# Kernel tuning notes

Measured on AMD Instinct MI355X. Metric: run time of the kernel, lower is better.

Reference implementation:

```python
import jax, jax.numpy as jnp
import numpy as np
from jax import lax

B, T = 64, 2048
ENC, DEC, ATT = 512, 1024, 128
NFILT, KSIZE = 32, 31
PAD = KSIZE // 2


def setup_inputs() -> dict:
    key = jax.random.key(0)
    ks = jax.random.split(key, 9)
    query = jax.random.normal(ks[0], (B, 1, DEC), dtype=jnp.float32)
    keys = jax.random.normal(ks[1], (B, T, ENC), dtype=jnp.float32)
    prev_weights = jax.random.uniform(ks[2], (B, T), dtype=jnp.float32)
    mask = jax.random.randint(ks[3], (B, T), 0, 2, dtype=jnp.int32)
    # params stored as [in, out] (transpose of torch Linear weight); same math
    W1 = jax.random.normal(ks[4], (ENC, ATT), dtype=jnp.float32) * (ENC ** -0.5)
    W2 = jax.random.normal(ks[5], (DEC, ATT), dtype=jnp.float32) * (DEC ** -0.5)
    V = jax.random.normal(ks[6], (ATT,), dtype=jnp.float32) * (ATT ** -0.5)
    conv_w = jax.random.normal(ks[7], (NFILT, 1, KSIZE), dtype=jnp.float32) * (KSIZE ** -0.5)
    loc_dense = jax.random.normal(ks[8], (NFILT, ATT), dtype=jnp.float32) * (NFILT ** -0.5)
    return {"query": query, "keys": keys, "prev_weights": prev_weights, "mask": mask,
            "W1": W1, "W2": W2, "V": V, "conv_w": conv_w, "loc_dense": loc_dense}


def reference(query, keys, prev_weights, mask, W1, W2, V, conv_w, loc_dense):
    proj_key = jnp.einsum('bte,ea->bta', keys, W1)          # [B,T,A]
    proj_query = jnp.einsum('bqd,da->bqa', query, W2)       # [B,1,A]
    # location conv: input [B,1,T], kernel [F,1,K], 'same' padding -> [B,F,T]
    loc_feat = lax.conv_general_dilated(prev_weights[:, None, :], conv_w,
                                        window_strides=(1,), padding=[(PAD, PAD)],
                                        dimension_numbers=('NCH', 'OIH', 'NCH'))
    proj_loc = jnp.einsum('bft,fa->bta', loc_feat, loc_dense)  # [B,T,A]
    scores = jnp.einsum('bta,a->bt', jnp.tanh(proj_key + proj_query + proj_loc), V)
    scores = jnp.where(mask == 0, -1e9, scores)
    weights = jax.nn.softmax(scores, axis=-1)                # [B,T]
    context = jnp.einsum('bt,bte->be', weights, keys)[:, None, :]  # [B,1,ENC]
    return context, weights
```

## Files before the change

kernel.cpp:

```cpp
#include <hip/hip_runtime.h>

typedef __attribute__((ext_vector_type(4))) float f32x4;
typedef __attribute__((ext_vector_type(8))) short bf16x8;

#define T_LEN 2048
#define ENC   512
#define DEC   1024
#define ATT   128
#define NB    64
#define BM    256
#define NTB   (T_LEN / BM)
#define NSTEP 17

typedef unsigned int u32;
typedef __attribute__((address_space(1))) const u32 gu32;
typedef __attribute__((address_space(3))) u32 lu32;

__device__ __forceinline__ void async_copy16(const void* g, void* l) {
  __builtin_amdgcn_global_load_lds((gu32*)g, (lu32*)l, 16, 0, 0);
}

__device__ __forceinline__ unsigned short f2bf_rne(float x) {
  unsigned int u = __builtin_bit_cast(unsigned int, x);
  u += 0x7fff + ((u >> 16) & 1);
  return (unsigned short)(u >> 16);
}
__device__ __forceinline__ short f2bf_fast(float x) {
  unsigned int u = __builtin_bit_cast(unsigned int, x);
  return (short)((u + 0x8000u) >> 16);
}

__device__ __forceinline__ float fast_tanh(float x) {
  float e = __expf(2.f * x);
  return 1.f - 2.f / (e + 1.f);
}

__global__ __launch_bounds__(128) void prep(
    const float* __restrict__ query, const float* __restrict__ W2,
    const float* __restrict__ W1, const float* __restrict__ convw,
    const float* __restrict__ ldense,
    float* __restrict__ pq, unsigned short* __restrict__ Bl) {
  int bidx = blockIdx.x;
  if (bidx < NB) {
    int a = threadIdx.x;
    const float* q = query + bidx * DEC;
    float a0 = 0.f, a1 = 0.f, a2 = 0.f, a3 = 0.f;
    for (int d = 0; d < DEC; d += 4) {
      a0 += q[d]     * W2[(d)     * ATT + a];
      a1 += q[d + 1] * W2[(d + 1) * ATT + a];
      a2 += q[d + 2] * W2[(d + 2) * ATT + a];
      a3 += q[d + 3] * W2[(d + 3) * ATT + a];
    }
    pq[bidx * ATT + a] = (a0 + a1) + (a2 + a3);
  } else {
    int a = bidx - NB;
    int n = a >> 4, rs = a & 15;
    for (int k = threadIdx.x; k < NSTEP * 32; k += 128) {
      float v = 0.f;
      if (k < 512) {
        v = W1[k * ATT + a];
      } else if (k < 543) {
        int kc = k - 512;
        #pragma unroll
        for (int f = 0; f < 32; ++f) v += convw[f * 31 + kc] * ldense[f * ATT + a];
      }
      int t = k >> 5, g = (k & 31) >> 3, j = k & 7;
      Bl[(((t * 8 + n) * 64 + g * 16 + rs) << 3) + j] = f2bf_rne(v);
    }
  }
}

__global__ __launch_bounds__(512, 2) void lsa_main(
    const float* __restrict__ keys, const float* __restrict__ prev,
    const int* __restrict__ mask, const unsigned short* __restrict__ Bl,
    const float* __restrict__ pq, const float* __restrict__ Vv,
    float* __restrict__ wout, float* __restrict__ dpart, float* __restrict__ cpart) {
  __shared__ unsigned short Bsh[NSTEP * 4096];
  __shared__ float e_vals[BM];

  const int tid = threadIdx.x;
  const int bid = blockIdx.x;
  const int b = bid >> 3;
  const int trow0 = (bid & 7) * BM;
  const int lane = tid & 63;
  const int w = tid >> 6;
  const int rsel = lane & 15, grp = lane >> 4;
  const int row0 = trow0 + w * 32;

  const float* keyrow = keys + ((size_t)b * T_LEN + row0 + rsel) * ENC + grp * 8;

  f32x4 acc[2][8];
  #pragma unroll
  for (int m = 0; m < 2; ++m)
    #pragma unroll
    for (int n = 0; n < 8; ++n) acc[m][n] = (f32x4)0.f;

  f32x4 aP[2][2], aQ[2][2];
  #pragma unroll
  for (int m = 0; m < 2; ++m) {
    aP[m][0] = *(const f32x4*)(keyrow + m * 16 * ENC);
    aP[m][1] = *(const f32x4*)(keyrow + m * 16 * ENC + 4);
  }
  {
    const char* src = (const char*)Bl + w * 1024 + lane * 16;
    char* dst = (char*)Bsh + w * 1024;
    #pragma unroll
    for (int s = 0; s < NSTEP; ++s)
      async_copy16(src + s * 8192, dst + s * 8192);
  }
  __syncthreads();

  #pragma unroll
  for (int t = 0; t < NSTEP; ++t) {
    f32x4 (&cur)[2][2] = (t & 1) ? aQ : aP;
    f32x4 (&nxt)[2][2] = (t & 1) ? aP : aQ;
    if (t < NSTEP - 2) {
      #pragma unroll
      for (int m = 0; m < 2; ++m) {
        nxt[m][0] = *(const f32x4*)(keyrow + m * 16 * ENC + (t + 1) * 32);
        nxt[m][1] = *(const f32x4*)(keyrow + m * 16 * ENC + (t + 1) * 32 + 4);
      }
    } else if (t == NSTEP - 2) {
      #pragma unroll
      for (int m = 0; m < 2; ++m)
        #pragma unroll
        for (int h = 0; h < 2; ++h)
          #pragma unroll
          for (int j = 0; j < 4; ++j) {
            int kk = grp * 8 + h * 4 + j;
            int pos = row0 + m * 16 + rsel + kk - 15;
            nxt[m][h][j] = (kk < 31 && pos >= 0 && pos < T_LEN) ? prev[b * T_LEN + pos] : 0.f;
          }
    }
    __builtin_amdgcn_sched_barrier(0);
    bf16x8 af[2];
    #pragma unroll
    for (int m = 0; m < 2; ++m)
      #pragma unroll
      for (int j = 0; j < 4; ++j) {
        af[m][j]     = f2bf_fast(cur[m][0][j]);
        af[m][4 + j] = f2bf_fast(cur[m][1][j]);
      }
    const unsigned short* Bt = &Bsh[t * 4096];
    #pragma unroll
    for (int n = 0; n < 8; ++n) {
      bf16x8 bf = *(const bf16x8*)(Bt + n * 512 + lane * 8);
      acc[0][n] = __builtin_amdgcn_mfma_f32_16x16x32_bf16(af[0], bf, acc[0][n], 0, 0, 0);
      acc[1][n] = __builtin_amdgcn_mfma_f32_16x16x32_bf16(af[1], bf, acc[1][n], 0, 0, 0);
    }
  }

  float psum[2][4];
  #pragma unroll
  for (int m = 0; m < 2; ++m)
    #pragma unroll
    for (int i = 0; i < 4; ++i) psum[m][i] = 0.f;
  #pragma unroll
  for (int n = 0; n < 8; ++n) {
    int c = n * 16 + rsel;
    float pqv = pq[b * ATT + c];
    float vv = Vv[c];
    #pragma unroll
    for (int m = 0; m < 2; ++m)
      #pragma unroll
      for (int i = 0; i < 4; ++i)
        psum[m][i] += vv * fast_tanh(acc[m][n][i] + pqv);
  }
  #pragma unroll
  for (int m = 0; m < 2; ++m)
    #pragma unroll
    for (int i = 0; i < 4; ++i) {
      float v = psum[m][i];
      v += __shfl_xor(v, 1, 64);
      v += __shfl_xor(v, 2, 64);
      v += __shfl_xor(v, 4, 64);
      v += __shfl_xor(v, 8, 64);
      psum[m][i] = v;
    }
  if (rsel == 0) {
    #pragma unroll
    for (int m = 0; m < 2; ++m)
      #pragma unroll
      for (int i = 0; i < 4; ++i) {
        int r = w * 32 + m * 16 + grp * 4 + i;
        int gr = b * T_LEN + trow0 + r;
        float e = (mask[gr] == 0) ? 0.f : __expf(psum[m][i]);
        wout[gr] = e;
        e_vals[r] = e;
      }
  }
  __syncthreads();

  if (tid < 64) {
    float v = e_vals[tid] + e_vals[tid + 64] + e_vals[tid + 128] + e_vals[tid + 192];
    #pragma unroll
    for (int off = 32; off; off >>= 1) v += __shfl_xor(v, off, 64);
    if (tid == 0) dpart[bid] = v;
  }

  {
    float c = 0.f;
    const float* kb = keys + ((size_t)b * T_LEN + trow0) * ENC + tid;
    #pragma unroll 16
    for (int r = 0; r < BM; ++r)
      c += e_vals[r] * kb[(size_t)r * ENC];
    cpart[(size_t)bid * ENC + tid] = c;
  }
}

__global__ __launch_bounds__(256) void lsa_finalize(
    const float* __restrict__ dpart, const float* __restrict__ cpart,
    float* __restrict__ out) {
  int b = blockIdx.x, tid = threadIdx.x;
  float d = 0.f;
  #pragma unroll
  for (int i = 0; i < NTB; ++i) d += dpart[b * NTB + i];
  float inv = 1.f / d;
  for (int e = tid; e < ENC; e += 256) {
    float c = 0.f;
    #pragma unroll
    for (int i = 0; i < NTB; ++i) c += cpart[((size_t)(b * NTB + i)) * ENC + e];
    out[b * ENC + e] = c * inv;
  }
  float* wrow = out + NB * ENC + (size_t)b * T_LEN;
  for (int t = tid; t < T_LEN; t += 256) wrow[t] *= inv;
}

extern "C" void kernel_launch(void* const* d_in, const int* in_sizes, int n_in,
                              void* d_out, int out_size, void* d_ws, size_t ws_size,
                              hipStream_t stream) {
  const float* query  = (const float*)d_in[0];
  const float* keys   = (const float*)d_in[1];
  const float* prev   = (const float*)d_in[2];
  const int*   mask   = (const int*)d_in[3];
  const float* W1     = (const float*)d_in[4];
  const float* W2     = (const float*)d_in[5];
  const float* V      = (const float*)d_in[6];
  const float* convw  = (const float*)d_in[7];
  const float* ldense = (const float*)d_in[8];
  float* out = (float*)d_out;

  char* ws = (char*)d_ws;
  unsigned short* Bl = (unsigned short*)ws;
  float* pq    = (float*)(ws + 139264);
  float* dpart = (float*)(ws + 139264 + 32768);
  float* cpart = (float*)(ws + 139264 + 32768 + 4096);

  prep<<<dim3(192), dim3(128), 0, stream>>>(query, W2, W1, convw, ldense, pq, Bl);
  lsa_main<<<dim3(NB * NTB), dim3(512), 0, stream>>>(keys, prev, mask, Bl, pq, V,
                                                     out + NB * ENC, dpart, cpart);
  lsa_finalize<<<dim3(NB), dim3(256), 0, stream>>>(dpart, cpart, out);
}
```

Baseline: 136.2 us.

## Triple-buffer key loads, drop sched barrier, split context accumulators

Replaces the double-buffered key register prefetch with a three-deep rotation (A/B/C), so loads are issued two steps ahead of the MFMA step that consumes them. The sched_barrier is removed and the min-blocks-per-CU hint drops from 2 to 1, which gives the compiler more register room. The context reduction loop is split into four independent accumulators to shorten its dependency chain. The cost is higher register pressure and possibly lower occupancy, which may reduce latency hiding across waves.

```diff
diff --git a/kernel.cpp b/kernel.cpp
--- a/kernel.cpp
+++ b/kernel.cpp
@@ -70,7 +70,7 @@
   }
 }
 
-__global__ __launch_bounds__(512, 2) void lsa_main(
+__global__ __launch_bounds__(512, 1) void lsa_main(
     const float* __restrict__ keys, const float* __restrict__ prev,
     const int* __restrict__ mask, const unsigned short* __restrict__ Bl,
     const float* __restrict__ pq, const float* __restrict__ Vv,
@@ -95,12 +95,42 @@
     #pragma unroll
     for (int n = 0; n < 8; ++n) acc[m][n] = (f32x4)0.f;
 
-  f32x4 aP[2][2], aQ[2][2];
-  #pragma unroll
-  for (int m = 0; m < 2; ++m) {
-    aP[m][0] = *(const f32x4*)(keyrow + m * 16 * ENC);
-    aP[m][1] = *(const f32x4*)(keyrow + m * 16 * ENC + 4);
-  }
+  f32x4 A0, A1, A2, A3, B0, B1, B2, B3, C0, C1, C2, C3;
+
+#define LOADK(S, t_) do { \
+    S##0 = *(const f32x4*)(keyrow + (t_) * 32); \
+    S##1 = *(const f32x4*)(keyrow + (t_) * 32 + 4); \
+    S##2 = *(const f32x4*)(keyrow + 16 * ENC + (t_) * 32); \
+    S##3 = *(const f32x4*)(keyrow + 16 * ENC + (t_) * 32 + 4); } while (0)
+
+#define LOADP(S) do { \
+    _Pragma("unroll") \
+    for (int j_ = 0; j_ < 4; ++j_) { \
+      int kk0 = grp * 8 + j_, kk1 = grp * 8 + 4 + j_; \
+      int p00 = row0 + rsel + kk0 - 15, p01 = row0 + rsel + kk1 - 15; \
+      S##0[j_] = (kk0 < 31 && p00 >= 0 && p00 < T_LEN) ? prev[b * T_LEN + p00] : 0.f; \
+      S##1[j_] = (kk1 < 31 && p01 >= 0 && p01 < T_LEN) ? prev[b * T_LEN + p01] : 0.f; \
+      S##2[j_] = (kk0 < 31 && p00 + 16 >= 0 && p00 + 16 < T_LEN) ? prev[b * T_LEN + p00 + 16] : 0.f; \
+      S##3[j_] = (kk1 < 31 && p01 + 16 >= 0 && p01 + 16 < T_LEN) ? prev[b * T_LEN + p01 + 16] : 0.f; \
+    } } while (0)
+
+#define STEP(t_, S) do { \
+    bf16x8 af0, af1; \
+    _Pragma("unroll") \
+    for (int j_ = 0; j_ < 4; ++j_) { \
+      af0[j_] = f2bf_fast(S##0[j_]); af0[4 + j_] = f2bf_fast(S##1[j_]); \
+      af1[j_] = f2bf_fast(S##2[j_]); af1[4 + j_] = f2bf_fast(S##3[j_]); \
+    } \
+    const unsigned short* Bt_ = &Bsh[(t_) * 4096]; \
+    _Pragma("unroll") \
+    for (int n_ = 0; n_ < 8; ++n_) { \
+      bf16x8 bf_ = *(const bf16x8*)(Bt_ + n_ * 512 + lane * 8); \
+      acc[0][n_] = __builtin_amdgcn_mfma_f32_16x16x32_bf16(af0, bf_, acc[0][n_], 0, 0, 0); \
+      acc[1][n_] = __builtin_amdgcn_mfma_f32_16x16x32_bf16(af1, bf_, acc[1][n_], 0, 0, 0); \
+    } } while (0)
+
+  LOADK(A, 0);
+  LOADK(B, 1);
   {
     const char* src = (const char*)Bl + w * 1024 + lane * 16;
     char* dst = (char*)Bsh + w * 1024;
@@ -110,45 +140,23 @@
   }
   __syncthreads();
 
-  #pragma unroll
-  for (int t = 0; t < NSTEP; ++t) {
-    f32x4 (&cur)[2][2] = (t & 1) ? aQ : aP;
-    f32x4 (&nxt)[2][2] = (t & 1) ? aP : aQ;
-    if (t < NSTEP - 2) {
-      #pragma unroll
-      for (int m = 0; m < 2; ++m) {
-        nxt[m][0] = *(const f32x4*)(keyrow + m * 16 * ENC + (t + 1) * 32);
-        nxt[m][1] = *(const f32x4*)(keyrow + m * 16 * ENC + (t + 1) * 32 + 4);
-      }
-    } else if (t == NSTEP - 2) {
-      #pragma unroll
-      for (int m = 0; m < 2; ++m)
-        #pragma unroll
-        for (int h = 0; h < 2; ++h)
-          #pragma unroll
-          for (int j = 0; j < 4; ++j) {
-            int kk = grp * 8 + h * 4 + j;
-            int pos = row0 + m * 16 + rsel + kk - 15;
-            nxt[m][h][j] = (kk < 31 && pos >= 0 && pos < T_LEN) ? prev[b * T_LEN + pos] : 0.f;
-          }
-    }
-    __builtin_amdgcn_sched_barrier(0);
-    bf16x8 af[2];
-    #pragma unroll
-    for (int m = 0; m < 2; ++m)
-      #pragma unroll
-      for (int j = 0; j < 4; ++j) {
-        af[m][j]     = f2bf_fast(cur[m][0][j]);
-        af[m][4 + j] = f2bf_fast(cur[m][1][j]);
-      }
-    const unsigned short* Bt = &Bsh[t * 4096];
-    #pragma unroll
-    for (int n = 0; n < 8; ++n) {
-      bf16x8 bf = *(const bf16x8*)(Bt + n * 512 + lane * 8);
-      acc[0][n] = __builtin_amdgcn_mfma_f32_16x16x32_bf16(af[0], bf, acc[0][n], 0, 0, 0);
-      acc[1][n] = __builtin_amdgcn_mfma_f32_16x16x32_bf16(af[1], bf, acc[1][n], 0, 0, 0);
-    }
-  }
+  LOADK(C, 2);  STEP(0, A);
+  LOADK(A, 3);  STEP(1, B);
+  LOADK(B, 4);  STEP(2, C);
+  LOADK(C, 5);  STEP(3, A);
+  LOADK(A, 6);  STEP(4, B);
+  LOADK(B, 7);  STEP(5, C);
+  LOADK(C, 8);  STEP(6, A);
+  LOADK(A, 9);  STEP(7, B);
+  LOADK(B, 10); STEP(8, C);
+  LOADK(C, 11); STEP(9, A);
+  LOADK(A, 12); STEP(10, B);
+  LOADK(B, 13); STEP(11, C);
+  LOADK(C, 14); STEP(12, A);
+  LOADK(A, 15); STEP(13, B);
+  LOADP(B);     STEP(14, C);
+  STEP(15, A);
+  STEP(16, B);
 
   float psum[2][4];
   #pragma unroll
@@ -199,12 +207,16 @@
   }
 
   {
-    float c = 0.f;
     const float* kb = keys + ((size_t)b * T_LEN + trow0) * ENC + tid;
-    #pragma unroll 16
-    for (int r = 0; r < BM; ++r)
-      c += e_vals[r] * kb[(size_t)r * ENC];
-    cpart[(size_t)bid * ENC + tid] = c;
+    float c0 = 0.f, c1 = 0.f, c2 = 0.f, c3 = 0.f;
+    #pragma unroll 4
+    for (int r = 0; r < BM; r += 4) {
+      c0 += e_vals[r]     * kb[(size_t)(r)     * ENC];
+      c1 += e_vals[r + 1] * kb[(size_t)(r + 1) * ENC];
+      c2 += e_vals[r + 2] * kb[(size_t)(r + 2) * ENC];
+      c3 += e_vals[r + 3] * kb[(size_t)(r + 3) * ENC];
+    }
+    cpart[(size_t)bid * ENC + tid] = (c0 + c1) + (c2 + c3);
   }
 }
 
```

New measurement: 137.4 us. About the same (+0.9%).
